# Performance work log

Hardware: AMD Instinct MI355X
Metric: run time of the kernel (lower is better)

The kernel has to match this reference:

```python
import jax, jax.numpy as jnp
import numpy as np

EPS = 1e-8  # torch CosineSimilarity default eps

def _normalize(x):
    # torch clamps each norm at eps before dividing
    n = jnp.sqrt(jnp.sum(x * x, axis=-1, keepdims=True))
    return x / jnp.maximum(n, EPS)

def _cross_entropy(logits, labels):
    logp = jax.nn.log_softmax(logits, axis=-1)
    return -jnp.mean(jnp.take_along_axis(logp, labels[:, None], axis=-1))

def setup_inputs() -> dict:
    key = jax.random.key(0)
    ks = jax.random.split(key, 7)
    B, M, D = 8192, 3129, 512
    return {
        'mm_proj': jax.random.normal(ks[0], (B, D), jnp.float32),
        'ans_embedding': jax.random.normal(ks[1], (M, D), jnp.float32),
        'v_max': jax.random.normal(ks[2], (B, D), jnp.float32),
        'mm': jax.random.normal(ks[3], (B, D), jnp.float32),
        'logits_q': jax.random.normal(ks[4], (B, M), jnp.float32),
        'logits_rubi': jax.random.normal(ks[5], (B, M), jnp.float32),
        'class_id': jax.random.randint(ks[6], (B, 1), 0, M, jnp.int64),
    }

def reference(mm_proj, ans_embedding, v_max, mm, logits_q, logits_rubi, class_id,
              question_loss_weight=1.0):
    cid = class_id.squeeze(1)  # [B]
    # NCE over cosine similarities: fuse normalize + GEMM instead of [B,M,D] expand
    g = _normalize(mm_proj)          # [B, D]
    a = _normalize(ans_embedding)    # [M, D]
    d_logit = jnp.einsum('bd,md->bm', g, a)  # [B, M] cosine matrix
    positive_dist = jnp.take_along_axis(d_logit, cid[:, None], axis=1)[:, 0]  # [B]
    num = jnp.exp(positive_dist)
    den = jnp.sum(jnp.exp(d_logit), axis=-1)
    loss_nce = jnp.mean(-jnp.log(num / den))
    # object cosine loss
    obj_dist = jnp.sum(_normalize(v_max) * _normalize(mm), axis=-1)  # [B]
    obj_loss = jnp.mean(1.0 - obj_dist)
    fusion_loss = (_cross_entropy(logits_rubi, cid) + obj_loss + loss_nce) / 3.0
    question_loss = _cross_entropy(logits_q, cid)
    loss = fusion_loss + question_loss_weight * question_loss
    # out['loss'], out['loss_mm_q'], out['loss_q']
    return jnp.stack([loss, fusion_loss, question_loss])
```

## Files before the change

### kernel.cpp

```cpp
#include <hip/hip_runtime.h>
#include <hip/hip_bf16.h>

#define B_N 8192
#define M_N 3129
#define M_PAD 3200
#define D_N 512

#define CE_L 12
#define CE_SPAN (CE_L * 256)
#define CE_WPA 8344
#define CE_WTOT (2 * CE_WPA)
#define CE_BLOCKS (CE_WTOT / 4)

#define GLOBAL_AS __attribute__((address_space(1)))
#define LDS_AS __attribute__((address_space(3)))

typedef __bf16 bf16x8 __attribute__((ext_vector_type(8)));
typedef float f32x4 __attribute__((ext_vector_type(4)));

#define PREP_G_BLOCKS   (B_N / 4)
#define PREP_A_BLOCKS   (M_PAD / 4)
#define PREP_OBJ_BLOCKS (B_N / 4)

__device__ __forceinline__ void normalize_row(
    const float* __restrict__ x, __bf16* __restrict__ y,
    int row, int nrows_src, int lane) {
  bf16x8 out;
  if (row >= nrows_src) {
    for (int j = 0; j < 8; ++j) out[j] = (__bf16)0.0f;
    *(bf16x8*)(y + (size_t)row * D_N + lane * 8) = out;
    return;
  }
  const float4* xr = (const float4*)(x + (size_t)row * D_N);
  float4 v0 = xr[lane * 2], v1 = xr[lane * 2 + 1];
  float s = v0.x*v0.x + v0.y*v0.y + v0.z*v0.z + v0.w*v0.w
          + v1.x*v1.x + v1.y*v1.y + v1.z*v1.z + v1.w*v1.w;
  for (int o = 1; o < 64; o <<= 1) s += __shfl_xor(s, o);
  float rn = 1.0f / fmaxf(sqrtf(s), 1e-8f);
  float vals[8] = {v0.x, v0.y, v0.z, v0.w, v1.x, v1.y, v1.z, v1.w};
  for (int j = 0; j < 8; ++j) out[j] = (__bf16)(vals[j] * rn);
  *(bf16x8*)(y + (size_t)row * D_N + lane * 8) = out;
}

__global__ __launch_bounds__(256) void prep_kernel(
    const float* __restrict__ mm_proj, const float* __restrict__ ans_emb,
    const float* __restrict__ v_max, const float* __restrict__ mm,
    __bf16* __restrict__ g, __bf16* __restrict__ a,
    float* __restrict__ obj) {
  int blk = blockIdx.x;
  int wid = threadIdx.x >> 6, lane = threadIdx.x & 63;
  if (blk < PREP_G_BLOCKS) {
    normalize_row(mm_proj, g, blk * 4 + wid, B_N, lane);
  } else if (blk < PREP_G_BLOCKS + PREP_A_BLOCKS) {
    normalize_row(ans_emb, a, (blk - PREP_G_BLOCKS) * 4 + wid, M_N, lane);
  } else {
    int b = (blk - PREP_G_BLOCKS - PREP_A_BLOCKS) * 4 + wid;
    const float4* vr = (const float4*)(v_max + (size_t)b * D_N);
    const float4* mr = (const float4*)(mm + (size_t)b * D_N);
    float4 a0 = vr[lane * 2], a1 = vr[lane * 2 + 1];
    float4 b0 = mr[lane * 2], b1 = mr[lane * 2 + 1];
    float sv = a0.x*a0.x + a0.y*a0.y + a0.z*a0.z + a0.w*a0.w
             + a1.x*a1.x + a1.y*a1.y + a1.z*a1.z + a1.w*a1.w;
    float sm = b0.x*b0.x + b0.y*b0.y + b0.z*b0.z + b0.w*b0.w
             + b1.x*b1.x + b1.y*b1.y + b1.z*b1.z + b1.w*b1.w;
    float sd = a0.x*b0.x + a0.y*b0.y + a0.z*b0.z + a0.w*b0.w
             + a1.x*b1.x + a1.y*b1.y + a1.z*b1.z + a1.w*b1.w;
    for (int o = 1; o < 64; o <<= 1) {
      sv += __shfl_xor(sv, o);
      sm += __shfl_xor(sm, o);
      sd += __shfl_xor(sd, o);
    }
    if (lane == 0) {
      float dist = sd / (fmaxf(sqrtf(sv), 1e-8f) * fmaxf(sqrtf(sm), 1e-8f));
      obj[b] = 1.0f - dist;
    }
  }
}

__global__ __launch_bounds__(256) void pos_kernel(
    const __bf16* __restrict__ g, const __bf16* __restrict__ a,
    const int* __restrict__ cid, float* __restrict__ pos) {
  int wid = threadIdx.x >> 6, lane = threadIdx.x & 63;
  int b = blockIdx.x * 4 + wid;
  if (b >= B_N) return;
  int label = cid[b];
  bf16x8 gv = *(const bf16x8*)(g + (size_t)b * D_N + lane * 8);
  bf16x8 av = *(const bf16x8*)(a + (size_t)label * D_N + lane * 8);
  float s = 0.0f;
  for (int j = 0; j < 8; ++j) s += (float)gv[j] * (float)av[j];
  for (int o = 1; o < 64; o <<= 1) s += __shfl_xor(s, o);
  if (lane == 0) pos[b] = s;
}

__global__ __launch_bounds__(256) void nce_gemm_kernel(
    const __bf16* __restrict__ g, const __bf16* __restrict__ a,
    float* __restrict__ den) {
  __shared__ __bf16 As[128 * 32];
  __shared__ __bf16 Bs[128 * 32];
  const int t = threadIdx.x;
  const int brow0 = blockIdx.y * 128;
  const int mrow0 = blockIdx.x * 128;
  const int lane = t & 63;
  const int wid = t >> 6;
  const int wrow = wid >> 1;
  const int wcol = wid & 1;
  const int r = lane & 15;
  const int quad = lane >> 4;

  f32x4 acc[4][4];
  for (int i = 0; i < 4; ++i)
    for (int j = 0; j < 4; ++j)
      acc[i][j] = f32x4{0.f, 0.f, 0.f, 0.f};

  for (int k0 = 0; k0 < D_N; k0 += 32) {
    __syncthreads();
    for (int i = 0; i < 2; ++i) {
      int s = t + i * 256;
      int row = s >> 2;
      int kq = (s & 3) << 3;
      const __bf16* ga = g + (size_t)(brow0 + row) * D_N + (k0 + kq);
      __builtin_amdgcn_global_load_lds((const GLOBAL_AS void*)ga,
                                       (LDS_AS void*)(As + s * 8), 16, 0, 0);
      const __bf16* gb = a + (size_t)(mrow0 + row) * D_N + (k0 + kq);
      __builtin_amdgcn_global_load_lds((const GLOBAL_AS void*)gb,
                                       (LDS_AS void*)(Bs + s * 8), 16, 0, 0);
    }
    __syncthreads();
    bf16x8 af[4], bf[4];
    for (int i = 0; i < 4; ++i)
      af[i] = *(const bf16x8*)(As + (wrow * 64 + i * 16 + r) * 32 + quad * 8);
    for (int j = 0; j < 4; ++j)
      bf[j] = *(const bf16x8*)(Bs + (wcol * 64 + j * 16 + r) * 32 + quad * 8);
    for (int i = 0; i < 4; ++i)
      for (int j = 0; j < 4; ++j)
        acc[i][j] = __builtin_amdgcn_mfma_f32_16x16x32_bf16(af[i], bf[j],
                                                            acc[i][j], 0, 0, 0);
  }

  for (int i = 0; i < 4; ++i) {
    for (int reg = 0; reg < 4; ++reg) {
      float s = 0.0f;
      for (int j = 0; j < 4; ++j) {
        int m = mrow0 + wcol * 64 + j * 16 + r;
        if (m < M_N) s += __expf(acc[i][j][reg]);
      }
      s += __shfl_xor(s, 1);
      s += __shfl_xor(s, 2);
      s += __shfl_xor(s, 4);
      s += __shfl_xor(s, 8);
      if (r == 0) {
        int b = brow0 + wrow * 64 + i * 16 + quad * 4 + reg;
        atomicAdd(den + b, s);
      }
    }
  }
}

__global__ __launch_bounds__(256) void ce_sum_kernel(
    const float* __restrict__ lq, const float* __restrict__ lr,
    float* __restrict__ rowsum) {
  const int lane = threadIdx.x & 63;
  const int gw = (int)((blockIdx.x * 256 + threadIdx.x) >> 6);
  const int aidx = (gw >= CE_WPA) ? 1 : 0;
  const unsigned wl = (unsigned)(gw - aidx * CE_WPA);
  const unsigned f0 = wl * (unsigned)CE_SPAN;
  const unsigned r0 = f0 / (unsigned)M_N;
  const unsigned b1 = (r0 + 1u) * (unsigned)M_N;
  const float* base = aidx ? lr : lq;
  const float* p = base + f0 + (unsigned)lane * 4u;

  float4 buf[6];
#pragma unroll
  for (int i = 0; i < 6; ++i) buf[i] = *(const float4*)(p + i * 256);

  float a0 = 0.f, a1 = 0.f;
  const unsigned fbase = f0 + (unsigned)lane * 4u;
#pragma unroll
  for (int i = 0; i < CE_L; ++i) {
    float4 v = buf[i % 6];
    if (i + 6 < CE_L) buf[i % 6] = *(const float4*)(p + (i + 6) * 256);
    unsigned f = fbase + (unsigned)i * 256u;
    float e0 = __expf(v.x), e1 = __expf(v.y), e2 = __expf(v.z), e3 = __expf(v.w);
    float lo = 0.f, hi = 0.f;
    if (f + 0u < b1) lo += e0; else hi += e0;
    if (f + 1u < b1) lo += e1; else hi += e1;
    if (f + 2u < b1) lo += e2; else hi += e2;
    if (f + 3u < b1) lo += e3; else hi += e3;
    a0 += lo; a1 += hi;
  }
  for (int o = 1; o < 64; o <<= 1) {
    a0 += __shfl_xor(a0, o);
    a1 += __shfl_xor(a1, o);
  }
  if (lane == 0) {
    float* rs = rowsum + (aidx ? B_N : 0);
    atomicAdd(rs + r0, a0);
    if (a1 != 0.f) atomicAdd(rs + r0 + 1, a1);
  }
}

__global__ __launch_bounds__(256) void final_reduce_kernel(
    const float* __restrict__ den, const float* __restrict__ pos,
    const float* __restrict__ rowsum,
    const float* __restrict__ lq, const float* __restrict__ lr,
    const int* __restrict__ cid, const float* __restrict__ obj,
    float* __restrict__ acc) {
  int b = blockIdx.x * 256 + threadIdx.x;
  int lab = cid[b];
  float xq = lq[(size_t)b * M_N + lab];
  float xr = lr[(size_t)b * M_N + lab];
  float s_nce = logf(den[b]) - pos[b];
  float s_ceq = logf(rowsum[b]) - xq;
  float s_cer = logf(rowsum[B_N + b]) - xr;
  float s_obj = obj[b];
  for (int o = 1; o < 64; o <<= 1) {
    s_nce += __shfl_xor(s_nce, o);
    s_ceq += __shfl_xor(s_ceq, o);
    s_cer += __shfl_xor(s_cer, o);
    s_obj += __shfl_xor(s_obj, o);
  }
  __shared__ float red[4][4];
  int wid = threadIdx.x >> 6;
  if ((threadIdx.x & 63) == 0) {
    red[wid][0] = s_nce; red[wid][1] = s_ceq;
    red[wid][2] = s_cer; red[wid][3] = s_obj;
  }
  __syncthreads();
  if (threadIdx.x < 4) {
    float v = red[0][threadIdx.x] + red[1][threadIdx.x]
            + red[2][threadIdx.x] + red[3][threadIdx.x];
    atomicAdd(acc + threadIdx.x, v);
  }
}

__global__ void final_combine_kernel(const float* __restrict__ acc,
                                     float* __restrict__ out) {
  if (threadIdx.x == 0) {
    float nce = acc[0] / (float)B_N;
    float ceq = acc[1] / (float)B_N;
    float cer = acc[2] / (float)B_N;
    float ob  = acc[3] / (float)B_N;
    float fusion = (cer + ob + nce) * (1.0f / 3.0f);
    out[0] = fusion + ceq;
    out[1] = fusion;
    out[2] = ceq;
  }
}

extern "C" void kernel_launch(void* const* d_in, const int* in_sizes, int n_in,
                              void* d_out, int out_size, void* d_ws, size_t ws_size,
                              hipStream_t stream) {
  const float* mm_proj     = (const float*)d_in[0];
  const float* ans_emb     = (const float*)d_in[1];
  const float* v_max       = (const float*)d_in[2];
  const float* mm          = (const float*)d_in[3];
  const float* logits_q    = (const float*)d_in[4];
  const float* logits_rubi = (const float*)d_in[5];
  const int*   cid         = (const int*)d_in[6];
  float* out = (float*)d_out;

  char* ws = (char*)d_ws;
  __bf16* g = (__bf16*)ws;
  __bf16* a = (__bf16*)(ws + 8388608);
  float* den    = (float*)(ws + 8388608 + 3276800);
  float* rowsum = den + B_N;
  float* acc    = rowsum + 2 * B_N;
  float* pos    = acc + 4;
  float* obj    = pos + B_N;

  hipMemsetAsync(den, 0, (size_t)(3 * B_N + 4) * sizeof(float), stream);

  prep_kernel<<<PREP_G_BLOCKS + PREP_A_BLOCKS + PREP_OBJ_BLOCKS, 256, 0,
                stream>>>(mm_proj, ans_emb, v_max, mm, g, a, obj);
  pos_kernel<<<B_N / 4, 256, 0, stream>>>(g, a, cid, pos);
  nce_gemm_kernel<<<dim3(M_PAD / 128, B_N / 128), 256, 0, stream>>>(g, a, den);
  ce_sum_kernel<<<CE_BLOCKS, 256, 0, stream>>>(logits_q, logits_rubi, rowsum);
  final_reduce_kernel<<<B_N / 256, 256, 0, stream>>>(den, pos, rowsum,
                                                     logits_q, logits_rubi,
                                                     cid, obj, acc);
  final_combine_kernel<<<1, 64, 0, stream>>>(acc, out);
}
```

Measured before the change: 329.7 us.

## Merge independent stages into two heterogeneous launches to overlap CE with prep and GEMM

```diff
diff --git a/kernel.cpp b/kernel.cpp
--- a/kernel.cpp
+++ b/kernel.cpp
@@ -10,17 +10,69 @@
 #define CE_SPAN (CE_L * 256)
 #define CE_WPA 8344
 #define CE_WTOT (2 * CE_WPA)
-#define CE_BLOCKS (CE_WTOT / 4)
-
-#define GLOBAL_AS __attribute__((address_space(1)))
-#define LDS_AS __attribute__((address_space(3)))
-
-typedef __bf16 bf16x8 __attribute__((ext_vector_type(8)));
-typedef float f32x4 __attribute__((ext_vector_type(4)));
+#define CE1_SPANS 10688
+#define CE2_SPANS (CE_WTOT - CE1_SPANS)
+#define CE1_BLOCKS (CE1_SPANS / 4)
+#define CE2_BLOCKS (CE2_SPANS / 4)
 
 #define PREP_G_BLOCKS   (B_N / 4)
 #define PREP_A_BLOCKS   (M_PAD / 4)
 #define PREP_OBJ_BLOCKS (B_N / 4)
+#define PREP_BLOCKS (PREP_G_BLOCKS + PREP_A_BLOCKS + PREP_OBJ_BLOCKS)
+
+#define GEMM_BLOCKS ((M_PAD / 128) * (B_N / 128))
+#define POS_BLOCKS  (B_N / 4)
+
+#define L1_BLOCKS (CE1_BLOCKS + PREP_BLOCKS)
+#define L2_BLOCKS (GEMM_BLOCKS + CE2_BLOCKS + POS_BLOCKS)
+
+#define GLOBAL_AS __attribute__((address_space(1)))
+#define LDS_AS __attribute__((address_space(3)))
+
+typedef __bf16 bf16x8 __attribute__((ext_vector_type(8)));
+typedef float f32x4 __attribute__((ext_vector_type(4)));
+
+__device__ __forceinline__ void ce_span(
+    int gw, const float* __restrict__ lq, const float* __restrict__ lr,
+    float* __restrict__ rowsum) {
+  const int lane = threadIdx.x & 63;
+  const int aidx = (gw >= CE_WPA) ? 1 : 0;
+  const unsigned wl = (unsigned)(gw - aidx * CE_WPA);
+  const unsigned f0 = wl * (unsigned)CE_SPAN;
+  const unsigned r0 = f0 / (unsigned)M_N;
+  const unsigned b1 = (r0 + 1u) * (unsigned)M_N;
+  const float* base = aidx ? lr : lq;
+  const float* p = base + f0 + (unsigned)lane * 4u;
+
+  float4 buf[6];
+#pragma unroll
+  for (int i = 0; i < 6; ++i) buf[i] = *(const float4*)(p + i * 256);
+
+  float a0 = 0.f, a1 = 0.f;
+  const unsigned fbase = f0 + (unsigned)lane * 4u;
+#pragma unroll
+  for (int i = 0; i < CE_L; ++i) {
+    float4 v = buf[i % 6];
+    if (i + 6 < CE_L) buf[i % 6] = *(const float4*)(p + (i + 6) * 256);
+    unsigned f = fbase + (unsigned)i * 256u;
+    float e0 = __expf(v.x), e1 = __expf(v.y), e2 = __expf(v.z), e3 = __expf(v.w);
+    float lo = 0.f, hi = 0.f;
+    if (f + 0u < b1) lo += e0; else hi += e0;
+    if (f + 1u < b1) lo += e1; else hi += e1;
+    if (f + 2u < b1) lo += e2; else hi += e2;
+    if (f + 3u < b1) lo += e3; else hi += e3;
+    a0 += lo; a1 += hi;
+  }
+  for (int o = 1; o < 64; o <<= 1) {
+    a0 += __shfl_xor(a0, o);
+    a1 += __shfl_xor(a1, o);
+  }
+  if (lane == 0) {
+    float* rs = rowsum + (aidx ? B_N : 0);
+    atomicAdd(rs + r0, a0);
+    if (a1 != 0.f) atomicAdd(rs + r0 + 1, a1);
+  }
+}
 
 __device__ __forceinline__ void normalize_row(
     const float* __restrict__ x, __bf16* __restrict__ y,
@@ -42,13 +94,19 @@
   *(bf16x8*)(y + (size_t)row * D_N + lane * 8) = out;
 }
 
-__global__ __launch_bounds__(256) void prep_kernel(
+__global__ __launch_bounds__(256) void l1_prep_ce_kernel(
     const float* __restrict__ mm_proj, const float* __restrict__ ans_emb,
     const float* __restrict__ v_max, const float* __restrict__ mm,
+    const float* __restrict__ lq, const float* __restrict__ lr,
     __bf16* __restrict__ g, __bf16* __restrict__ a,
-    float* __restrict__ obj) {
+    float* __restrict__ obj, float* __restrict__ rowsum) {
   int blk = blockIdx.x;
   int wid = threadIdx.x >> 6, lane = threadIdx.x & 63;
+  if (blk < CE1_BLOCKS) {
+    ce_span(blk * 4 + wid, lq, lr, rowsum);
+    return;
+  }
+  blk -= CE1_BLOCKS;
   if (blk < PREP_G_BLOCKS) {
     normalize_row(mm_proj, g, blk * 4 + wid, B_N, lane);
   } else if (blk < PREP_G_BLOCKS + PREP_A_BLOCKS) {
@@ -77,125 +135,109 @@
   }
 }
 
-__global__ __launch_bounds__(256) void pos_kernel(
+__global__ __launch_bounds__(256) void l2_gemm_ce_pos_kernel(
     const __bf16* __restrict__ g, const __bf16* __restrict__ a,
-    const int* __restrict__ cid, float* __restrict__ pos) {
-  int wid = threadIdx.x >> 6, lane = threadIdx.x & 63;
-  int b = blockIdx.x * 4 + wid;
-  if (b >= B_N) return;
-  int label = cid[b];
-  bf16x8 gv = *(const bf16x8*)(g + (size_t)b * D_N + lane * 8);
-  bf16x8 av = *(const bf16x8*)(a + (size_t)label * D_N + lane * 8);
-  float s = 0.0f;
-  for (int j = 0; j < 8; ++j) s += (float)gv[j] * (float)av[j];
-  for (int o = 1; o < 64; o <<= 1) s += __shfl_xor(s, o);
-  if (lane == 0) pos[b] = s;
-}
-
-__global__ __launch_bounds__(256) void nce_gemm_kernel(
-    const __bf16* __restrict__ g, const __bf16* __restrict__ a,
-    float* __restrict__ den) {
+    const int* __restrict__ cid,
+    const float* __restrict__ mm_proj, const float* __restrict__ ans_emb,
+    const float* __restrict__ lq, const float* __restrict__ lr,
+    float* __restrict__ den, float* __restrict__ pos,
+    float* __restrict__ rowsum) {
   __shared__ __bf16 As[128 * 32];
   __shared__ __bf16 Bs[128 * 32];
+  int blk = blockIdx.x;
   const int t = threadIdx.x;
-  const int brow0 = blockIdx.y * 128;
-  const int mrow0 = blockIdx.x * 128;
   const int lane = t & 63;
   const int wid = t >> 6;
-  const int wrow = wid >> 1;
-  const int wcol = wid & 1;
-  const int r = lane & 15;
-  const int quad = lane >> 4;
-
-  f32x4 acc[4][4];
-  for (int i = 0; i < 4; ++i)
-    for (int j = 0; j < 4; ++j)
-      acc[i][j] = f32x4{0.f, 0.f, 0.f, 0.f};
-
-  for (int k0 = 0; k0 < D_N; k0 += 32) {
-    __syncthreads();
-    for (int i = 0; i < 2; ++i) {
-      int s = t + i * 256;
-      int row = s >> 2;
-      int kq = (s & 3) << 3;
-      const __bf16* ga = g + (size_t)(brow0 + row) * D_N + (k0 + kq);
-      __builtin_amdgcn_global_load_lds((const GLOBAL_AS void*)ga,
-                                       (LDS_AS void*)(As + s * 8), 16, 0, 0);
-      const __bf16* gb = a + (size_t)(mrow0 + row) * D_N + (k0 + kq);
-      __builtin_amdgcn_global_load_lds((const GLOBAL_AS void*)gb,
-                                       (LDS_AS void*)(Bs + s * 8), 16, 0, 0);
-    }
-    __syncthreads();
-    bf16x8 af[4], bf[4];
-    for (int i = 0; i < 4; ++i)
-      af[i] = *(const bf16x8*)(As + (wrow * 64 + i * 16 + r) * 32 + quad * 8);
-    for (int j = 0; j < 4; ++j)
-      bf[j] = *(const bf16x8*)(Bs + (wcol * 64 + j * 16 + r) * 32 + quad * 8);
+
+  if (blk < GEMM_BLOCKS) {
+    const int brow0 = (blk / (M_PAD / 128)) * 128;
+    const int mrow0 = (blk % (M_PAD / 128)) * 128;
+    const int wrow = wid >> 1;
+    const int wcol = wid & 1;
+    const int r = lane & 15;
+    const int quad = lane >> 4;
+
+    f32x4 acc[4][4];
     for (int i = 0; i < 4; ++i)
       for (int j = 0; j < 4; ++j)
-        acc[i][j] = __builtin_amdgcn_mfma_f32_16x16x32_bf16(af[i], bf[j],
-                                                            acc[i][j], 0, 0, 0);
-  }
-
-  for (int i = 0; i < 4; ++i) {
-    for (int reg = 0; reg < 4; ++reg) {
-      float s = 0.0f;
-      for (int j = 0; j < 4; ++j) {
-        int m = mrow0 + wcol * 64 + j * 16 + r;
-        if (m < M_N) s += __expf(acc[i][j][reg]);
+        acc[i][j] = f32x4{0.f, 0.f, 0.f, 0.f};
+
+    for (int k0 = 0; k0 < D_N; k0 += 32) {
+      __syncthreads();
+      for (int i = 0; i < 2; ++i) {
+        int s = t + i * 256;
+        int row = s >> 2;
+        int kq = (s & 3) << 3;
+        const __bf16* ga = g + (size_t)(brow0 + row) * D_N + (k0 + kq);
+        __builtin_amdgcn_global_load_lds((const GLOBAL_AS void*)ga,
+                                         (LDS_AS void*)(As + s * 8), 16, 0, 0);
+        const __bf16* gb = a + (size_t)(mrow0 + row) * D_N + (k0 + kq);
+        __builtin_amdgcn_global_load_lds((const GLOBAL_AS void*)gb,
+                                         (LDS_AS void*)(Bs + s * 8), 16, 0, 0);
       }
-      s += __shfl_xor(s, 1);
-      s += __shfl_xor(s, 2);
-      s += __shfl_xor(s, 4);
-      s += __shfl_xor(s, 8);
-      if (r == 0) {
-        int b = brow0 + wrow * 64 + i * 16 + quad * 4 + reg;
-        atomicAdd(den + b, s);
+      __syncthreads();
+      bf16x8 af[4], bf[4];
+      for (int i = 0; i < 4; ++i)
+        af[i] = *(const bf16x8*)(As + (wrow * 64 + i * 16 + r) * 32 + quad * 8);
+      for (int j = 0; j < 4; ++j)
+        bf[j] = *(const bf16x8*)(Bs + (wcol * 64 + j * 16 + r) * 32 + quad * 8);
+      for (int i = 0; i < 4; ++i)
+        for (int j = 0; j < 4; ++j)
+          acc[i][j] = __builtin_amdgcn_mfma_f32_16x16x32_bf16(af[i], bf[j],
+                                                              acc[i][j], 0, 0, 0);
+    }
+
+    for (int i = 0; i < 4; ++i) {
+      for (int reg = 0; reg < 4; ++reg) {
+        float s = 0.0f;
+        for (int j = 0; j < 4; ++j) {
+          int m = mrow0 + wcol * 64 + j * 16 + r;
+          if (m < M_N) s += __expf(acc[i][j][reg]);
+        }
+        s += __shfl_xor(s, 1);
+        s += __shfl_xor(s, 2);
+        s += __shfl_xor(s, 4);
+        s += __shfl_xor(s, 8);
+        if (r == 0) {
+          int b = brow0 + wrow * 64 + i * 16 + quad * 4 + reg;
+          atomicAdd(den + b, s);
+        }
       }
     }
-  }
-}
-
-__global__ __launch_bounds__(256) void ce_sum_kernel(
-    const float* __restrict__ lq, const float* __restrict__ lr,
-    float* __restrict__ rowsum) {
-  const int lane = threadIdx.x & 63;
-  const int gw = (int)((blockIdx.x * 256 + threadIdx.x) >> 6);
-  const int aidx = (gw >= CE_WPA) ? 1 : 0;
-  const unsigned wl = (unsigned)(gw - aidx * CE_WPA);
-  const unsigned f0 = wl * (unsigned)CE_SPAN;
-  const unsigned r0 = f0 / (unsigned)M_N;
-  const unsigned b1 = (r0 + 1u) * (unsigned)M_N;
-  const float* base = aidx ? lr : lq;
-  const float* p = base + f0 + (unsigned)lane * 4u;
-
-  float4 buf[6];
-#pragma unroll
-  for (int i = 0; i < 6; ++i) buf[i] = *(const float4*)(p + i * 256);
-
-  float a0 = 0.f, a1 = 0.f;
-  const unsigned fbase = f0 + (unsigned)lane * 4u;
-#pragma unroll
-  for (int i = 0; i < CE_L; ++i) {
-    float4 v = buf[i % 6];
-    if (i + 6 < CE_L) buf[i % 6] = *(const float4*)(p + (i + 6) * 256);
-    unsigned f = fbase + (unsigned)i * 256u;
-    float e0 = __expf(v.x), e1 = __expf(v.y), e2 = __expf(v.z), e3 = __expf(v.w);
-    float lo = 0.f, hi = 0.f;
-    if (f + 0u < b1) lo += e0; else hi += e0;
-    if (f + 1u < b1) lo += e1; else hi += e1;
-    if (f + 2u < b1) lo += e2; else hi += e2;
-    if (f + 3u < b1) lo += e3; else hi += e3;
-    a0 += lo; a1 += hi;
-  }
-  for (int o = 1; o < 64; o <<= 1) {
-    a0 += __shfl_xor(a0, o);
-    a1 += __shfl_xor(a1, o);
-  }
-  if (lane == 0) {
-    float* rs = rowsum + (aidx ? B_N : 0);
-    atomicAdd(rs + r0, a0);
-    if (a1 != 0.f) atomicAdd(rs + r0 + 1, a1);
+    return;
+  }
+  blk -= GEMM_BLOCKS;
+
+  if (blk < CE2_BLOCKS) {
+    ce_span(CE1_SPANS + blk * 4 + wid, lq, lr, rowsum);
+    return;
+  }
+  blk -= CE2_BLOCKS;
+
+  {
+    int b = blk * 4 + wid;
+    int label = cid[b];
+    const float4* xr = (const float4*)(mm_proj + (size_t)b * D_N);
+    float4 v0 = xr[lane * 2], v1 = xr[lane * 2 + 1];
+    const float4* yr = (const float4*)(ans_emb + (size_t)label * D_N);
+    float4 w0 = yr[lane * 2], w1 = yr[lane * 2 + 1];
+    float sg = v0.x*v0.x + v0.y*v0.y + v0.z*v0.z + v0.w*v0.w
+             + v1.x*v1.x + v1.y*v1.y + v1.z*v1.z + v1.w*v1.w;
+    float sa = w0.x*w0.x + w0.y*w0.y + w0.z*w0.z + w0.w*w0.w
+             + w1.x*w1.x + w1.y*w1.y + w1.z*w1.z + w1.w*w1.w;
+    for (int o = 1; o < 64; o <<= 1) {
+      sg += __shfl_xor(sg, o);
+      sa += __shfl_xor(sa, o);
+    }
+    float rng = 1.0f / fmaxf(sqrtf(sg), 1e-8f);
+    float rna = 1.0f / fmaxf(sqrtf(sa), 1e-8f);
+    float gv[8] = {v0.x, v0.y, v0.z, v0.w, v1.x, v1.y, v1.z, v1.w};
+    float av[8] = {w0.x, w0.y, w0.z, w0.w, w1.x, w1.y, w1.z, w1.w};
+    float d = 0.0f;
+    for (int j = 0; j < 8; ++j)
+      d += (float)(__bf16)(gv[j] * rng) * (float)(__bf16)(av[j] * rna);
+    for (int o = 1; o < 64; o <<= 1) d += __shfl_xor(d, o);
+    if (lane == 0) pos[b] = d;
   }
 }
 
@@ -270,11 +312,10 @@
 
   hipMemsetAsync(den, 0, (size_t)(3 * B_N + 4) * sizeof(float), stream);
 
-  prep_kernel<<<PREP_G_BLOCKS + PREP_A_BLOCKS + PREP_OBJ_BLOCKS, 256, 0,
-                stream>>>(mm_proj, ans_emb, v_max, mm, g, a, obj);
-  pos_kernel<<<B_N / 4, 256, 0, stream>>>(g, a, cid, pos);
-  nce_gemm_kernel<<<dim3(M_PAD / 128, B_N / 128), 256, 0, stream>>>(g, a, den);
-  ce_sum_kernel<<<CE_BLOCKS, 256, 0, stream>>>(logits_q, logits_rubi, rowsum);
+  l1_prep_ce_kernel<<<L1_BLOCKS, 256, 0, stream>>>(
+      mm_proj, ans_emb, v_max, mm, logits_q, logits_rubi, g, a, obj, rowsum);
+  l2_gemm_ce_pos_kernel<<<L2_BLOCKS, 256, 0, stream>>>(
+      g, a, cid, mm_proj, ans_emb, logits_q, logits_rubi, den, pos, rowsum);
   final_reduce_kernel<<<B_N / 256, 256, 0, stream>>>(den, pos, rowsum,
                                                      logits_q, logits_rubi,
                                                      cid, obj, acc);
```

Measured after the change: 319.4 us. 3.1% less time.
